# Performance work log

Measured on AMD Instinct MI355X. Metric: run time of the kernel, lower is better.

The kernel has to match this reference:

```python
import jax, jax.numpy as jnp
import numpy as np

# dims
B, S, D, DS = 4, 4096, 2048, 64
NF, NR, NT = 4096, 2048, 2048  # feature / relational / transfer neuron pools
KF, KR, KT = 8, 4, 6           # top-k per pool


def setup_inputs() -> dict:
    key = jax.random.key(0)
    k1, k2, k3, k4 = jax.random.split(key, 4)
    x = jax.random.normal(k1, (B, S, D), dtype=jnp.float32)
    importance = jax.random.uniform(k2, (B, S), dtype=jnp.float32)
    proj_w = jax.random.normal(k3, (D, DS), dtype=jnp.float32) * 0.02
    proj_b = jnp.zeros((DS,), dtype=jnp.float32)
    neuron_emb = jax.random.normal(k4, (NF + NR + NT, DS), dtype=jnp.float32) * 0.02
    return {"x": x, "importance": importance, "proj_w": proj_w,
            "proj_b": proj_b, "neuron_emb": neuron_emb}


def _topk_sparsify(w, k):
    # top-k along last dim, scatter back, renormalize (matches _topk_sparsify)
    vals, idx = jax.lax.top_k(w, k)                      # [B,k]
    rows = jnp.arange(w.shape[0])[:, None]
    sparse = jnp.zeros_like(w).at[rows, idx].set(vals)   # [B,N]
    return sparse / (sparse.sum(axis=-1, keepdims=True) + 1e-8)


def reference(x, importance, proj_w, proj_b, neuron_emb):
    # eval mode: dropout off, no excitability bias, no aux loss
    h = x @ proj_w + proj_b                               # [B,S,DS]
    norm = jnp.maximum(jnp.linalg.norm(neuron_emb, axis=-1, keepdims=True), 1e-12)
    emb = neuron_emb / norm                               # F.normalize
    logits = jnp.einsum('bsd,nd->bsn', h, emb)            # [B,S,NF+NR+NT]

    feat_pref = jax.nn.softmax(logits[..., :NF], axis=-1)
    relQ_pref = jax.nn.softmax(logits[..., NF:NF + NR], axis=-1)
    relK_pref = jax.nn.softmax(logits[..., NF:NF + NR], axis=-1)
    tran_pref = jax.nn.softmax(logits[..., NF + NR:], axis=-1)

    # importance-weighted pooling over tokens -> dense per-batch routing weights
    fw = _topk_sparsify(jnp.einsum('bs,bsn->bn', importance, feat_pref), KF)
    qw = _topk_sparsify(jnp.einsum('bs,bsn->bn', importance, relQ_pref), KR)
    kw = _topk_sparsify(jnp.einsum('bs,bsn->bn', importance, relK_pref), KR)
    tw = _topk_sparsify(jnp.einsum('bs,bsn->bn', importance, tran_pref), KT)

    return jnp.concatenate([fw, qw, kw, tw], axis=-1)     # [B, NF+2*NR+NT]
```

## Files before the change

### kernel.cpp

```cpp
#include <hip/hip_runtime.h>
#include <math.h>

#define BATCH 4
#define SEQ   4096
#define DIM   2048
#define DS    64
#define NF    4096
#define NR    2048
#define NT    2048
#define NTOT  8192
#define TOK   16384
#define KSPLIT 8
#define KS    (DIM / KSPLIT)

typedef __attribute__((ext_vector_type(8))) __bf16 bf16x8;
typedef __attribute__((ext_vector_type(4))) float  f32x4;

static __device__ __forceinline__ unsigned short f2bf(float x) {
  unsigned int u = __float_as_uint(x);
  u += 0x7fffu + ((u >> 16) & 1u);
  return (unsigned short)(u >> 16);
}
static __device__ __forceinline__ float bf2f(unsigned int lo16) {
  return __uint_as_float(lo16 << 16);
}

static __device__ __forceinline__ void split8(const float4& a, const float4& b,
                                              bf16x8& hi, bf16x8& lo) {
  float v[8] = {a.x, a.y, a.z, a.w, b.x, b.y, b.z, b.w};
  union { unsigned short u[8]; bf16x8 v8; } H, L;
#pragma unroll
  for (int i = 0; i < 8; ++i) {
    unsigned short h = f2bf(v[i]);
    H.u[i] = h;
    L.u[i] = f2bf(v[i] - bf2f(h));
  }
  hi = H.v8; lo = L.v8;
}

__global__ __launch_bounds__(256) void k_prep_emb(const float* __restrict__ emb,
                                                  unsigned short* __restrict__ eh,
                                                  unsigned short* __restrict__ el) {
  int row  = blockIdx.x * 4 + (threadIdx.x >> 6);
  int lane = threadIdx.x & 63;
  float v  = emb[(size_t)row * DS + lane];
  float ss = v * v;
#pragma unroll
  for (int m = 32; m >= 1; m >>= 1) ss += __shfl_xor(ss, m, 64);
  float sc = 1.0f / fmaxf(sqrtf(ss), 1e-12f);
  float w  = v * sc;
  unsigned short hi = f2bf(w);
  eh[(size_t)row * DS + lane] = hi;
  el[(size_t)row * DS + lane] = f2bf(w - bf2f(hi));
}

__global__ __launch_bounds__(256) void k_prep_w(const float* __restrict__ W,
                                                unsigned short* __restrict__ wth,
                                                unsigned short* __restrict__ wtl) {
  int c = blockIdx.x;
#pragma unroll
  for (int it = 0; it < 8; ++it) {
    int k = threadIdx.x + it * 256;
    float v = W[(size_t)k * DS + c];
    unsigned short hi = f2bf(v);
    wth[(size_t)c * DIM + k] = hi;
    wtl[(size_t)c * DIM + k] = f2bf(v - bf2f(hi));
  }
}

__global__ __launch_bounds__(512) void k_h(
    const float* __restrict__ x, const unsigned short* __restrict__ wth,
    const unsigned short* __restrict__ wtl, float* __restrict__ Hpart) {
  __shared__ __align__(16) unsigned short wsh[64 * KS];
  __shared__ __align__(16) unsigned short wsl[64 * KS];
  const int tid   = threadIdx.x;
  const int t0    = blockIdx.x * 128;
  const int kbase = blockIdx.y * KS;
  const int lane  = tid & 63, wv = tid >> 6;
  const int fr    = lane & 15, oct = lane >> 4;

#pragma unroll
  for (int it = 0; it < 4; ++it) {
    int idx = tid + it * 512;
    int c = idx >> 5, k16 = idx & 31;
    int bo = (c * 512 + k16 * 16) ^ ((c & 7) << 4);
    size_t src = ((size_t)c * DIM + kbase) * 2 + (size_t)k16 * 16;
    *reinterpret_cast<uint4*>((char*)wsh + bo) =
        *reinterpret_cast<const uint4*>((const char*)wth + src);
    *reinterpret_cast<uint4*>((char*)wsl + bo) =
        *reinterpret_cast<const uint4*>((const char*)wtl + src);
  }
  __syncthreads();

  const float* xp = x + (size_t)(t0 + wv * 16 + fr) * DIM + kbase + oct * 8;

  f32x4 acc[4];
#pragma unroll
  for (int j = 0; j < 4; ++j) acc[j] = (f32x4)0.0f;

  float4 xa = *reinterpret_cast<const float4*>(xp);
  float4 xb = *reinterpret_cast<const float4*>(xp + 4);

#pragma unroll
  for (int s = 0; s < KS / 32; ++s) {
    bf16x8 ah, al;
    split8(xa, xb, ah, al);
    if (s + 1 < KS / 32) {
      xa = *reinterpret_cast<const float4*>(xp + (s + 1) * 32);
      xb = *reinterpret_cast<const float4*>(xp + (s + 1) * 32 + 4);
    }
#pragma unroll
    for (int j = 0; j < 4; ++j) {
      int col = j * 16 + fr;
      int bo = (col * 512 + s * 64 + oct * 16) ^ ((col & 7) << 4);
      bf16x8 bh = *reinterpret_cast<const bf16x8*>((const char*)wsh + bo);
      bf16x8 bl = *reinterpret_cast<const bf16x8*>((const char*)wsl + bo);
      acc[j] = __builtin_amdgcn_mfma_f32_16x16x32_bf16(ah, bh, acc[j], 0, 0, 0);
      acc[j] = __builtin_amdgcn_mfma_f32_16x16x32_bf16(ah, bl, acc[j], 0, 0, 0);
      acc[j] = __builtin_amdgcn_mfma_f32_16x16x32_bf16(al, bh, acc[j], 0, 0, 0);
    }
  }

  float* op = Hpart + (size_t)blockIdx.y * TOK * DS;
#pragma unroll
  for (int j = 0; j < 4; ++j) {
    int c = j * 16 + fr;
#pragma unroll
    for (int r = 0; r < 4; ++r) {
      int t = t0 + wv * 16 + oct * 4 + r;
      op[(size_t)t * DS + c] = acc[j][r];
    }
  }
}

__global__ __launch_bounds__(256) void k_hc(const float* __restrict__ Hpart,
                                            const float* __restrict__ bias,
                                            unsigned short* __restrict__ hh,
                                            unsigned short* __restrict__ hl) {
  int idx = blockIdx.x * 256 + threadIdx.x;
  int t = idx >> 4, q = idx & 15;
  size_t o = (size_t)t * DS + q * 4;
  float4 bv = *reinterpret_cast<const float4*>(&bias[q * 4]);
  float v0 = bv.x, v1 = bv.y, v2 = bv.z, v3 = bv.w;
#pragma unroll
  for (int p = 0; p < KSPLIT; ++p) {
    float4 s = *reinterpret_cast<const float4*>(&Hpart[(size_t)p * TOK * DS + o]);
    v0 += s.x; v1 += s.y; v2 += s.z; v3 += s.w;
  }
  unsigned short h0 = f2bf(v0), h1 = f2bf(v1), h2 = f2bf(v2), h3 = f2bf(v3);
  uint2 hi; hi.x = h0 | ((unsigned)h1 << 16); hi.y = h2 | ((unsigned)h3 << 16);
  uint2 lo;
  lo.x = (unsigned)f2bf(v0 - bf2f(h0)) | ((unsigned)f2bf(v1 - bf2f(h1)) << 16);
  lo.y = (unsigned)f2bf(v2 - bf2f(h2)) | ((unsigned)f2bf(v3 - bf2f(h3)) << 16);
  *reinterpret_cast<uint2*>(&hh[o]) = hi;
  *reinterpret_cast<uint2*>(&hl[o]) = lo;
}

template<int MODE>
__global__ __launch_bounds__(256, 3) void k_zle(
    const unsigned short* __restrict__ hh, const unsigned short* __restrict__ hl,
    const unsigned short* __restrict__ eh, const unsigned short* __restrict__ el,
    const float* __restrict__ a, float* __restrict__ Zp, float* __restrict__ Bp) {
  __shared__ __align__(16) unsigned short esh[128 * 64];
  __shared__ __align__(16) unsigned short esl[128 * 64];
  __shared__ float red2[512];
  const int tid = threadIdx.x;
  const int tb  = blockIdx.x;
  const int cb  = blockIdx.y;
  const int t0  = tb * 128;

  const int lane = tid & 63;
  const int wv   = tid >> 6;
  const int fr   = lane & 15;
  const int oct  = lane >> 4;

  bf16x8 ah[2][2], al[2][2];
#pragma unroll
  for (int i = 0; i < 2; ++i)
#pragma unroll
    for (int kh = 0; kh < 2; ++kh) {
      size_t off = (size_t)(t0 + wv * 32 + i * 16 + fr) * DS + kh * 32 + oct * 8;
      ah[i][kh] = *reinterpret_cast<const bf16x8*>(hh + off);
      al[i][kh] = *reinterpret_cast<const bf16x8*>(hl + off);
    }

  float av[2][4];
  if (MODE == 2) {
    const int sl = (cb < 8) ? 0 : ((cb < 12) ? 1 : 2);
#pragma unroll
    for (int i = 0; i < 2; ++i)
#pragma unroll
      for (int r = 0; r < 4; ++r)
        av[i][r] = a[(size_t)sl * TOK + t0 + wv * 32 + i * 16 + oct * 4 + r];
  }
  float rs[2][4];
#pragma unroll
  for (int i = 0; i < 2; ++i)
#pragma unroll
    for (int r = 0; r < 4; ++r) rs[i][r] = 0.0f;

  for (int sub = 0; sub < 4; ++sub) {
    const int n0 = cb * 512 + sub * 128;
    if (sub) __syncthreads();
#pragma unroll
    for (int it = 0; it < 4; ++it) {
      int idx = tid + it * 256;
      int r = idx >> 3, k8 = idx & 7;
      int bo = (r * 128 + k8 * 16) ^ ((r & 7) << 4);
      *reinterpret_cast<uint4*>((char*)esh + bo) =
          *reinterpret_cast<const uint4*>((const char*)eh + (size_t)(n0 + r) * 128 + k8 * 16);
      *reinterpret_cast<uint4*>((char*)esl + bo) =
          *reinterpret_cast<const uint4*>((const char*)el + (size_t)(n0 + r) * 128 + k8 * 16);
    }
    __syncthreads();

    f32x4 acc[2][8];
#pragma unroll
    for (int i = 0; i < 2; ++i)
#pragma unroll
      for (int j = 0; j < 8; ++j) acc[i][j] = (f32x4)0.0f;

#pragma unroll
    for (int j = 0; j < 8; ++j) {
      int col = j * 16 + fr;
      bf16x8 bh[2], bl[2];
#pragma unroll
      for (int kh = 0; kh < 2; ++kh) {
        int bo = (col * 128 + (kh * 32 + oct * 8) * 2) ^ ((col & 7) << 4);
        bh[kh] = *reinterpret_cast<const bf16x8*>((const char*)esh + bo);
        bl[kh] = *reinterpret_cast<const bf16x8*>((const char*)esl + bo);
      }
#pragma unroll
      for (int i = 0; i < 2; ++i) {
#pragma unroll
        for (int kh = 0; kh < 2; ++kh) {
          acc[i][j] = __builtin_amdgcn_mfma_f32_16x16x32_bf16(ah[i][kh], bh[kh], acc[i][j], 0, 0, 0);
          acc[i][j] = __builtin_amdgcn_mfma_f32_16x16x32_bf16(ah[i][kh], bl[kh], acc[i][j], 0, 0, 0);
          acc[i][j] = __builtin_amdgcn_mfma_f32_16x16x32_bf16(al[i][kh], bh[kh], acc[i][j], 0, 0, 0);
        }
      }
    }

    if (MODE == 0) {
#pragma unroll
      for (int i = 0; i < 2; ++i)
#pragma unroll
        for (int j = 0; j < 8; ++j)
#pragma unroll
          for (int r = 0; r < 4; ++r) rs[i][r] += __expf(acc[i][j][r]);
    } else {
      float cs[8];
#pragma unroll
      for (int j = 0; j < 8; ++j) {
        float s = 0.0f;
#pragma unroll
        for (int i = 0; i < 2; ++i)
#pragma unroll
          for (int r = 0; r < 4; ++r) s = fmaf(av[i][r], __expf(acc[i][j][r]), s);
        cs[j] = s;
      }
#pragma unroll
      for (int j = 0; j < 8; ++j) {
        cs[j] += __shfl_xor(cs[j], 16, 64);
        cs[j] += __shfl_xor(cs[j], 32, 64);
      }
      if (oct == 0) {
#pragma unroll
        for (int j = 0; j < 8; ++j) red2[wv * 128 + j * 16 + fr] = cs[j];
      }
      __syncthreads();
      if (tid < 128) {
        float v = red2[tid] + red2[128 + tid] + red2[256 + tid] + red2[384 + tid];
        Bp[(size_t)tb * NTOT + n0 + tid] = v;
      }
    }
  }

  if (MODE == 0) {
#pragma unroll
    for (int m = 1; m < 16; m <<= 1)
#pragma unroll
      for (int i = 0; i < 2; ++i)
#pragma unroll
        for (int r = 0; r < 4; ++r) rs[i][r] += __shfl_xor(rs[i][r], m, 64);
    if (fr == 0) {
#pragma unroll
      for (int i = 0; i < 2; ++i)
#pragma unroll
        for (int r = 0; r < 4; ++r) {
          int t = t0 + wv * 32 + i * 16 + oct * 4 + r;
          Zp[(size_t)t * 16 + cb] = rs[i][r];
        }
    }
  }
}

__global__ __launch_bounds__(256) void k_a2(const float* __restrict__ Zp,
                                            const float* __restrict__ imp,
                                            float* __restrict__ a) {
  int t = blockIdx.x * 256 + threadIdx.x;
  const float4* zp = reinterpret_cast<const float4*>(&Zp[(size_t)t * 16]);
  float4 q0 = zp[0], q1 = zp[1], q2 = zp[2], q3 = zp[3];
  float zf = ((q0.x + q0.y) + (q0.z + q0.w)) + ((q1.x + q1.y) + (q1.z + q1.w));
  float zr = (q2.x + q2.y) + (q2.z + q2.w);
  float zt = (q3.x + q3.y) + (q3.z + q3.w);
  float im = imp[t];
  a[t]           = im / zf;
  a[TOK + t]     = im / zr;
  a[2 * TOK + t] = im / zt;
}

__global__ __launch_bounds__(256) void k_red(const float* __restrict__ Bp,
                                             float* __restrict__ pooled) {
  int idx = blockIdx.x * 256 + threadIdx.x;
  int b = idx >> 13;
  int n = idx & (NTOT - 1);
  const float* src = Bp + (size_t)(b * 32) * NTOT + n;
  float s = 0.0f;
#pragma unroll
  for (int g = 0; g < 32; ++g) s += src[(size_t)g * NTOT];
  pooled[idx] = s;
}

__global__ __launch_bounds__(256) void k_topk(const float* __restrict__ pooled,
                                              float* __restrict__ out) {
  __shared__ float p[4096];
  __shared__ float rv[256];
  __shared__ int   ri[256];
  __shared__ float vals[8];
  __shared__ int   idxs[8];
  __shared__ float s_inv;

  const int bid = blockIdx.x;
  const int b   = bid / 3;
  const int sl  = bid % 3;
  const int off = (sl == 0) ? 0 : ((sl == 1) ? NF : NF + NR);
  const int N   = (sl == 0) ? NF : NR;
  const int K   = (sl == 0) ? 8 : ((sl == 1) ? 4 : 6);
  const int tid = threadIdx.x;

  for (int i = tid; i < N; i += 256)
    p[i] = pooled[(size_t)b * NTOT + off + i];
  __syncthreads();

  for (int k = 0; k < K; ++k) {
    float bv = -2.0f;
    int bi = 1 << 30;
    for (int i = tid; i < N; i += 256) {
      float v = p[i];
      if (v > bv) { bv = v; bi = i; }
    }
    rv[tid] = bv; ri[tid] = bi;
    __syncthreads();
    for (int st = 128; st > 0; st >>= 1) {
      if (tid < st) {
        float v2 = rv[tid + st]; int i2 = ri[tid + st];
        if (v2 > rv[tid] || (v2 == rv[tid] && i2 < ri[tid])) {
          rv[tid] = v2; ri[tid] = i2;
        }
      }
      __syncthreads();
    }
    if (tid == 0) {
      vals[k] = rv[0]; idxs[k] = ri[0];
      p[ri[0]] = -1.0f;
    }
    __syncthreads();
  }

  if (tid == 0) {
    float s = 0.0f;
    for (int k = 0; k < K; ++k) s += vals[k];
    s_inv = 1.0f / (s + 1e-8f);
  }
  __syncthreads();

  float* ob = out + (size_t)b * (NF + 2 * NR + NT);
  if (sl == 0) {
    for (int i = tid; i < NF; i += 256) ob[i] = 0.0f;
  } else if (sl == 1) {
    for (int i = tid; i < NR; i += 256) { ob[NF + i] = 0.0f; ob[NF + NR + i] = 0.0f; }
  } else {
    for (int i = tid; i < NT; i += 256) ob[NF + 2 * NR + i] = 0.0f;
  }
  __syncthreads();
  if (tid < K) {
    float v = vals[tid] * s_inv;
    int ix = idxs[tid];
    if (sl == 0) {
      ob[ix] = v;
    } else if (sl == 1) {
      ob[NF + ix] = v;
      ob[NF + NR + ix] = v;
    } else {
      ob[NF + 2 * NR + ix] = v;
    }
  }
}

extern "C" void kernel_launch(void* const* d_in, const int* in_sizes, int n_in,
                              void* d_out, int out_size, void* d_ws, size_t ws_size,
                              hipStream_t stream) {
  const float* x    = (const float*)d_in[0];
  const float* imp  = (const float*)d_in[1];
  const float* W    = (const float*)d_in[2];
  const float* bias = (const float*)d_in[3];
  const float* emb  = (const float*)d_in[4];
  float* out = (float*)d_out;

  unsigned short* eh  = (unsigned short*)d_ws;
  unsigned short* el  = eh  + (size_t)NTOT * DS;
  unsigned short* wth = el  + (size_t)NTOT * DS;
  unsigned short* wtl = wth + (size_t)DS * DIM;
  unsigned short* hh  = wtl + (size_t)DS * DIM;
  unsigned short* hl  = hh  + (size_t)TOK * DS;
  float* Zp     = (float*)(hl + (size_t)TOK * DS);
  float* a      = Zp + (size_t)TOK * 16;
  float* Bp     = a + 3 * (size_t)TOK;
  float* pooled = Bp + (size_t)128 * NTOT;
  float* Hpart  = pooled + (size_t)BATCH * NTOT;

  size_t need = (2 * (size_t)NTOT * DS + 2 * (size_t)DS * DIM +
                 2 * (size_t)TOK * DS) * sizeof(unsigned short) +
                ((size_t)TOK * 16 + 3 * (size_t)TOK + 128 * (size_t)NTOT +
                 (size_t)BATCH * NTOT + (size_t)KSPLIT * TOK * DS) * sizeof(float);
  if (ws_size < need) return;

  k_prep_emb<<<NTOT / 4, 256, 0, stream>>>(emb, eh, el);
  k_prep_w<<<DS, 256, 0, stream>>>(W, wth, wtl);
  k_h<<<dim3(TOK / 128, KSPLIT), 512, 0, stream>>>(x, wth, wtl, Hpart);
  k_hc<<<TOK * 16 / 256, 256, 0, stream>>>(Hpart, bias, hh, hl);

  k_zle<0><<<dim3(128, 16), 256, 0, stream>>>(hh, hl, eh, el, nullptr, Zp, nullptr);
  k_a2<<<TOK / 256, 256, 0, stream>>>(Zp, imp, a);
  k_zle<2><<<dim3(128, 16), 256, 0, stream>>>(hh, hl, eh, el, a, nullptr, Bp);
  k_red<<<(BATCH * NTOT) / 256, 256, 0, stream>>>(Bp, pooled);
  k_topk<<<12, 256, 0, stream>>>(pooled, out);
}
```

Baseline: 170.0 us.

## Retile logits kernels: keep 256-neuron embedding tile resident, loop over tokens

The two logits passes now load a 256-neuron slice of the split-bf16 embedding into shared memory once per block and iterate over 512 tokens, instead of loading 128-token activations and streaming four 128-neuron embedding sub-tiles. Pooled partial sums stay in registers across token iterations, so per-subtile block barriers and Bp writes disappear and the downstream reduction handles 8 rather than 32 partials. The cost is twice the shared memory, occupancy lowered from 3 to 2 blocks per CU, and a wider Zp layout (32 partial sums per token).

Result: slower. 300.4 us (+76.7%).

```diff
diff --git a/kernel.cpp b/kernel.cpp
--- a/kernel.cpp
+++ b/kernel.cpp
@@ -157,141 +157,152 @@
 }
 
 template<int MODE>
-__global__ __launch_bounds__(256, 3) void k_zle(
+__global__ __launch_bounds__(256, 2) void k_zle(
     const unsigned short* __restrict__ hh, const unsigned short* __restrict__ hl,
     const unsigned short* __restrict__ eh, const unsigned short* __restrict__ el,
     const float* __restrict__ a, float* __restrict__ Zp, float* __restrict__ Bp) {
-  __shared__ __align__(16) unsigned short esh[128 * 64];
-  __shared__ __align__(16) unsigned short esl[128 * 64];
-  __shared__ float red2[512];
+  __shared__ __align__(16) unsigned short esh[256 * 64];
+  __shared__ __align__(16) unsigned short esl[256 * 64];
+  __shared__ float red2[1024];
   const int tid = threadIdx.x;
-  const int tb  = blockIdx.x;
-  const int cb  = blockIdx.y;
-  const int t0  = tb * 128;
+  const int cb  = blockIdx.x;
+  const int tg  = blockIdx.y;
+  const int n0  = cb * 256;
+
+#pragma unroll
+  for (int it = 0; it < 8; ++it) {
+    int idx = tid + it * 256;
+    int r = idx >> 3, k8 = idx & 7;
+    int bo = (r * 128 + k8 * 16) ^ ((r & 7) << 4);
+    *reinterpret_cast<uint4*>((char*)esh + bo) =
+        *reinterpret_cast<const uint4*>((const char*)eh + (size_t)(n0 + r) * 128 + k8 * 16);
+    *reinterpret_cast<uint4*>((char*)esl + bo) =
+        *reinterpret_cast<const uint4*>((const char*)el + (size_t)(n0 + r) * 128 + k8 * 16);
+  }
+  __syncthreads();
 
   const int lane = tid & 63;
   const int wv   = tid >> 6;
   const int fr   = lane & 15;
   const int oct  = lane >> 4;
-
-  bf16x8 ah[2][2], al[2][2];
-#pragma unroll
-  for (int i = 0; i < 2; ++i)
-#pragma unroll
-    for (int kh = 0; kh < 2; ++kh) {
-      size_t off = (size_t)(t0 + wv * 32 + i * 16 + fr) * DS + kh * 32 + oct * 8;
-      ah[i][kh] = *reinterpret_cast<const bf16x8*>(hh + off);
-      al[i][kh] = *reinterpret_cast<const bf16x8*>(hl + off);
-    }
-
-  float av[2][4];
-  if (MODE == 2) {
-    const int sl = (cb < 8) ? 0 : ((cb < 12) ? 1 : 2);
+  const int sl   = (cb < 16) ? 0 : ((cb < 24) ? 1 : 2);
+
+  float pool[16];
+#pragma unroll
+  for (int j = 0; j < 16; ++j) pool[j] = 0.0f;
+
+#pragma unroll 1
+  for (int it = 0; it < 4; ++it) {
+    const int tbase = tg * 512 + it * 128 + wv * 32;
+
+    bf16x8 ah[2][2], al[2][2];
 #pragma unroll
     for (int i = 0; i < 2; ++i)
 #pragma unroll
-      for (int r = 0; r < 4; ++r)
-        av[i][r] = a[(size_t)sl * TOK + t0 + wv * 32 + i * 16 + oct * 4 + r];
-  }
-  float rs[2][4];
-#pragma unroll
-  for (int i = 0; i < 2; ++i)
-#pragma unroll
-    for (int r = 0; r < 4; ++r) rs[i][r] = 0.0f;
-
-  for (int sub = 0; sub < 4; ++sub) {
-    const int n0 = cb * 512 + sub * 128;
-    if (sub) __syncthreads();
-#pragma unroll
-    for (int it = 0; it < 4; ++it) {
-      int idx = tid + it * 256;
-      int r = idx >> 3, k8 = idx & 7;
-      int bo = (r * 128 + k8 * 16) ^ ((r & 7) << 4);
-      *reinterpret_cast<uint4*>((char*)esh + bo) =
-          *reinterpret_cast<const uint4*>((const char*)eh + (size_t)(n0 + r) * 128 + k8 * 16);
-      *reinterpret_cast<uint4*>((char*)esl + bo) =
-          *reinterpret_cast<const uint4*>((const char*)el + (size_t)(n0 + r) * 128 + k8 * 16);
-    }
-    __syncthreads();
-
-    f32x4 acc[2][8];
-#pragma unroll
-    for (int i = 0; i < 2; ++i)
-#pragma unroll
-      for (int j = 0; j < 8; ++j) acc[i][j] = (f32x4)0.0f;
-
-#pragma unroll
-    for (int j = 0; j < 8; ++j) {
-      int col = j * 16 + fr;
-      bf16x8 bh[2], bl[2];
-#pragma unroll
       for (int kh = 0; kh < 2; ++kh) {
-        int bo = (col * 128 + (kh * 32 + oct * 8) * 2) ^ ((col & 7) << 4);
-        bh[kh] = *reinterpret_cast<const bf16x8*>((const char*)esh + bo);
-        bl[kh] = *reinterpret_cast<const bf16x8*>((const char*)esl + bo);
+        size_t off = (size_t)(tbase + i * 16 + fr) * DS + kh * 32 + oct * 8;
+        ah[i][kh] = *reinterpret_cast<const bf16x8*>(hh + off);
+        al[i][kh] = *reinterpret_cast<const bf16x8*>(hl + off);
       }
-#pragma unroll
-      for (int i = 0; i < 2; ++i) {
+
+    float av[2][4];
+    if (MODE == 2) {
+#pragma unroll
+      for (int i = 0; i < 2; ++i)
+#pragma unroll
+        for (int r = 0; r < 4; ++r)
+          av[i][r] = a[(size_t)sl * TOK + tbase + i * 16 + oct * 4 + r];
+    }
+    float rs[2][4];
+    if (MODE == 0) {
+#pragma unroll
+      for (int i = 0; i < 2; ++i)
+#pragma unroll
+        for (int r = 0; r < 4; ++r) rs[i][r] = 0.0f;
+    }
+
+#pragma unroll
+    for (int jh = 0; jh < 2; ++jh) {
+      f32x4 acc[2][8];
+#pragma unroll
+      for (int i = 0; i < 2; ++i)
+#pragma unroll
+        for (int j = 0; j < 8; ++j) acc[i][j] = (f32x4)0.0f;
+
+#pragma unroll
+      for (int j = 0; j < 8; ++j) {
+        int col = (jh * 8 + j) * 16 + fr;
+        bf16x8 bh[2], bl[2];
 #pragma unroll
         for (int kh = 0; kh < 2; ++kh) {
-          acc[i][j] = __builtin_amdgcn_mfma_f32_16x16x32_bf16(ah[i][kh], bh[kh], acc[i][j], 0, 0, 0);
-          acc[i][j] = __builtin_amdgcn_mfma_f32_16x16x32_bf16(ah[i][kh], bl[kh], acc[i][j], 0, 0, 0);
-          acc[i][j] = __builtin_amdgcn_mfma_f32_16x16x32_bf16(al[i][kh], bh[kh], acc[i][j], 0, 0, 0);
+          int bo = (col * 128 + (kh * 32 + oct * 8) * 2) ^ ((col & 7) << 4);
+          bh[kh] = *reinterpret_cast<const bf16x8*>((const char*)esh + bo);
+          bl[kh] = *reinterpret_cast<const bf16x8*>((const char*)esl + bo);
+        }
+#pragma unroll
+        for (int i = 0; i < 2; ++i) {
+#pragma unroll
+          for (int kh = 0; kh < 2; ++kh) {
+            acc[i][j] = __builtin_amdgcn_mfma_f32_16x16x32_bf16(ah[i][kh], bh[kh], acc[i][j], 0, 0, 0);
+            acc[i][j] = __builtin_amdgcn_mfma_f32_16x16x32_bf16(ah[i][kh], bl[kh], acc[i][j], 0, 0, 0);
+            acc[i][j] = __builtin_amdgcn_mfma_f32_16x16x32_bf16(al[i][kh], bh[kh], acc[i][j], 0, 0, 0);
+          }
         }
       }
+
+      if (MODE == 0) {
+#pragma unroll
+        for (int i = 0; i < 2; ++i)
+#pragma unroll
+          for (int j = 0; j < 8; ++j)
+#pragma unroll
+            for (int r = 0; r < 4; ++r) rs[i][r] += __expf(acc[i][j][r]);
+      } else {
+#pragma unroll
+        for (int j = 0; j < 8; ++j) {
+          float s = 0.0f;
+#pragma unroll
+          for (int i = 0; i < 2; ++i)
+#pragma unroll
+            for (int r = 0; r < 4; ++r)
+              s = fmaf(av[i][r], __expf(acc[i][j][r]), s);
+          pool[jh * 8 + j] += s;
+        }
+      }
     }
 
     if (MODE == 0) {
 #pragma unroll
-      for (int i = 0; i < 2; ++i)
-#pragma unroll
-        for (int j = 0; j < 8; ++j)
-#pragma unroll
-          for (int r = 0; r < 4; ++r) rs[i][r] += __expf(acc[i][j][r]);
-    } else {
-      float cs[8];
-#pragma unroll
-      for (int j = 0; j < 8; ++j) {
-        float s = 0.0f;
+      for (int m = 1; m < 16; m <<= 1)
 #pragma unroll
         for (int i = 0; i < 2; ++i)
 #pragma unroll
-          for (int r = 0; r < 4; ++r) s = fmaf(av[i][r], __expf(acc[i][j][r]), s);
-        cs[j] = s;
+          for (int r = 0; r < 4; ++r) rs[i][r] += __shfl_xor(rs[i][r], m, 64);
+      if (fr == 0) {
+#pragma unroll
+        for (int i = 0; i < 2; ++i)
+#pragma unroll
+          for (int r = 0; r < 4; ++r) {
+            int t = tbase + i * 16 + oct * 4 + r;
+            Zp[(size_t)t * 32 + cb] = rs[i][r];
+          }
       }
-#pragma unroll
-      for (int j = 0; j < 8; ++j) {
-        cs[j] += __shfl_xor(cs[j], 16, 64);
-        cs[j] += __shfl_xor(cs[j], 32, 64);
-      }
-      if (oct == 0) {
-#pragma unroll
-        for (int j = 0; j < 8; ++j) red2[wv * 128 + j * 16 + fr] = cs[j];
-      }
-      __syncthreads();
-      if (tid < 128) {
-        float v = red2[tid] + red2[128 + tid] + red2[256 + tid] + red2[384 + tid];
-        Bp[(size_t)tb * NTOT + n0 + tid] = v;
-      }
-    }
-  }
-
-  if (MODE == 0) {
-#pragma unroll
-    for (int m = 1; m < 16; m <<= 1)
-#pragma unroll
-      for (int i = 0; i < 2; ++i)
-#pragma unroll
-        for (int r = 0; r < 4; ++r) rs[i][r] += __shfl_xor(rs[i][r], m, 64);
-    if (fr == 0) {
-#pragma unroll
-      for (int i = 0; i < 2; ++i)
-#pragma unroll
-        for (int r = 0; r < 4; ++r) {
-          int t = t0 + wv * 32 + i * 16 + oct * 4 + r;
-          Zp[(size_t)t * 16 + cb] = rs[i][r];
-        }
-    }
+    }
+  }
+
+  if (MODE == 2) {
+#pragma unroll
+    for (int j = 0; j < 16; ++j) {
+      pool[j] += __shfl_xor(pool[j], 16, 64);
+      pool[j] += __shfl_xor(pool[j], 32, 64);
+    }
+    if (oct == 0) {
+#pragma unroll
+      for (int j = 0; j < 16; ++j) red2[wv * 256 + j * 16 + fr] = pool[j];
+    }
+    __syncthreads();
+    float v = red2[tid] + red2[256 + tid] + red2[512 + tid] + red2[768 + tid];
+    Bp[(size_t)tg * NTOT + n0 + tid] = v;
   }
 }
 
@@ -299,11 +310,14 @@
                                             const float* __restrict__ imp,
                                             float* __restrict__ a) {
   int t = blockIdx.x * 256 + threadIdx.x;
-  const float4* zp = reinterpret_cast<const float4*>(&Zp[(size_t)t * 16]);
-  float4 q0 = zp[0], q1 = zp[1], q2 = zp[2], q3 = zp[3];
-  float zf = ((q0.x + q0.y) + (q0.z + q0.w)) + ((q1.x + q1.y) + (q1.z + q1.w));
-  float zr = (q2.x + q2.y) + (q2.z + q2.w);
-  float zt = (q3.x + q3.y) + (q3.z + q3.w);
+  const float4* zp = reinterpret_cast<const float4*>(&Zp[(size_t)t * 32]);
+  float zf = 0.f, zr = 0.f, zt = 0.f;
+#pragma unroll
+  for (int q = 0; q < 4; ++q) { float4 v = zp[q]; zf += (v.x + v.y) + (v.z + v.w); }
+#pragma unroll
+  for (int q = 4; q < 6; ++q) { float4 v = zp[q]; zr += (v.x + v.y) + (v.z + v.w); }
+#pragma unroll
+  for (int q = 6; q < 8; ++q) { float4 v = zp[q]; zt += (v.x + v.y) + (v.z + v.w); }
   float im = imp[t];
   a[t]           = im / zf;
   a[TOK + t]     = im / zr;
@@ -315,10 +329,10 @@
   int idx = blockIdx.x * 256 + threadIdx.x;
   int b = idx >> 13;
   int n = idx & (NTOT - 1);
-  const float* src = Bp + (size_t)(b * 32) * NTOT + n;
+  const float* src = Bp + (size_t)(b * 8) * NTOT + n;
   float s = 0.0f;
 #pragma unroll
-  for (int g = 0; g < 32; ++g) s += src[(size_t)g * NTOT];
+  for (int g = 0; g < 8; ++g) s += src[(size_t)g * NTOT];
   pooled[idx] = s;
 }
 
@@ -415,14 +429,14 @@
   unsigned short* hh  = wtl + (size_t)DS * DIM;
   unsigned short* hl  = hh  + (size_t)TOK * DS;
   float* Zp     = (float*)(hl + (size_t)TOK * DS);
-  float* a      = Zp + (size_t)TOK * 16;
+  float* a      = Zp + (size_t)TOK * 32;
   float* Bp     = a + 3 * (size_t)TOK;
-  float* pooled = Bp + (size_t)128 * NTOT;
+  float* pooled = Bp + (size_t)32 * NTOT;
   float* Hpart  = pooled + (size_t)BATCH * NTOT;
 
   size_t need = (2 * (size_t)NTOT * DS + 2 * (size_t)DS * DIM +
                  2 * (size_t)TOK * DS) * sizeof(unsigned short) +
-                ((size_t)TOK * 16 + 3 * (size_t)TOK + 128 * (size_t)NTOT +
+                ((size_t)TOK * 32 + 3 * (size_t)TOK + 32 * (size_t)NTOT +
                  (size_t)BATCH * NTOT + (size_t)KSPLIT * TOK * DS) * sizeof(float);
   if (ws_size < need) return;
 
@@ -431,9 +445,9 @@
   k_h<<<dim3(TOK / 128, KSPLIT), 512, 0, stream>>>(x, wth, wtl, Hpart);
   k_hc<<<TOK * 16 / 256, 256, 0, stream>>>(Hpart, bias, hh, hl);
 
-  k_zle<0><<<dim3(128, 16), 256, 0, stream>>>(hh, hl, eh, el, nullptr, Zp, nullptr);
+  k_zle<0><<<dim3(32, 32), 256, 0, stream>>>(hh, hl, eh, el, nullptr, Zp, nullptr);
   k_a2<<<TOK / 256, 256, 0, stream>>>(Zp, imp, a);
-  k_zle<2><<<dim3(128, 16), 256, 0, stream>>>(hh, hl, eh, el, a, nullptr, Bp);
+  k_zle<2><<<dim3(32, 32), 256, 0, stream>>>(hh, hl, eh, el, a, nullptr, Bp);
   k_red<<<(BATCH * NTOT) / 256, 256, 0, stream>>>(Bp, pooled);
   k_topk<<<12, 256, 0, stream>>>(pooled, out);
 }
```
